# Performance work log

Hardware: AMD Instinct MI355X
Metric: run time of the kernel (lower is better)

## Reference

```python
import jax, jax.numpy as jnp
import numpy as np

B, C, H, W = 4, 16, 512, 512
OUT = 16
HID = 64
EPS = 1e-5


def _ln(x, g, b):
    mu = x.mean(-1, keepdims=True)
    v = x.var(-1, keepdims=True)
    return (x - mu) / jnp.sqrt(v + EPS) * g + b


def setup_inputs() -> dict:
    key = jax.random.key(0)
    ks = jax.random.split(key, 8)
    HW = H * W
    d = {}
    d['input'] = jax.random.normal(ks[0], (B, C, H, W), jnp.float32)
    d['W1'] = jax.random.normal(ks[1], (HID, HW), jnp.float32) * 0.01   # Linear1 weight [64, HW]
    d['b1'] = jnp.zeros((HID,), jnp.float32)
    d['ln1_g'] = jnp.ones((HID,), jnp.float32)
    d['ln1_b'] = jnp.zeros((HID,), jnp.float32)
    d['W2'] = jax.random.normal(ks[2], (HW, HID), jnp.float32) * 0.02   # Linear2 weight [HW, 64]
    d['b2'] = jnp.zeros((HW,), jnp.float32)
    d['ln2_g'] = jnp.ones((HW,), jnp.float32)
    d['ln2_b'] = jnp.zeros((HW,), jnp.float32)
    d['cw1'] = jax.random.normal(ks[3], (1, C, 1, 1), jnp.float32) * 0.1   # 1x1 conv C->1
    d['cb1'] = jnp.zeros((1,), jnp.float32)
    d['cw3'] = jax.random.normal(ks[4], (OUT, C, 3, 3), jnp.float32) * 0.05  # 3x3 conv C->OUT
    d['cb3'] = jnp.zeros((OUT,), jnp.float32)
    d['bn_g'] = jnp.ones((OUT,), jnp.float32)
    d['bn_b'] = jnp.zeros((OUT,), jnp.float32)
    return d


def reference(input, W1, b1, ln1_g, ln1_b, W2, b2, ln2_g, ln2_b, cw1, cb1, cw3, cb3, bn_g, bn_b):
    Bq, Cq, Hq, Wq = input.shape
    HW = Hq * Wq
    m = input.reshape(Bq, Cq, HW)
    # Linear1 -> LN -> ReLU  (per-channel over flattened spatial dim)
    h = jax.nn.relu(_ln(m @ W1.T + b1, ln1_g, ln1_b))            # [B, C, 64]
    # Linear2 -> LN -> ReLU
    m2 = jax.nn.relu(_ln(h @ W2.T + b2, ln2_g, ln2_b))           # [B, C, HW]
    m2 = m2.reshape(Bq, Cq, Hq, Wq)
    # 1x1 conv C -> 1
    score = jnp.einsum('bchw,oc->bohw', m2, cw1[:, :, 0, 0]) + cb1[:, None, None]  # [B,1,H,W]
    # keep_topk: ratio 0.25, no grad
    K = HW // 4
    flat = jax.lax.stop_gradient(score.reshape(Bq, HW))
    _, idx = jax.lax.top_k(flat, K)                               # [B, K]
    mask = jnp.zeros_like(flat).at[jnp.arange(Bq)[:, None], idx].set(1.0).reshape(Bq, 1, Hq, Wq)
    # boolean-mask gather: torch selects in ascending flat-index order
    idx_s = jnp.sort(idx, axis=1)                                 # [B, K]
    g = jnp.take_along_axis(m, idx_s[:, None, :], axis=2).reshape(Bq, Cq, Hq // 2, Wq // 2)
    # out_conv: 3x3 conv -> BatchNorm (batch stats, training mode) -> ReLU
    y = jax.lax.conv_general_dilated(g, cw3, (1, 1), [(1, 1), (1, 1)],
                                     dimension_numbers=('NCHW', 'OIHW', 'NCHW'))
    y = y + cb3[:, None, None]
    mu = y.mean((0, 2, 3), keepdims=True)
    v = y.var((0, 2, 3), keepdims=True)
    y = jax.nn.relu((y - mu) / jnp.sqrt(v + EPS) * bn_g[:, None, None] + bn_b[:, None, None])
    return (y, mask)
```

## Files before the change

kernel.cpp:

```cpp
#include <hip/hip_runtime.h>

#define HWN    262144
#define KSEL   65536
#define TIECAP 2048

#define OFF_H      0
#define OFF_DOT1   32768
#define OFF_G      65536
#define OFF_WBAR   98304
#define OFF_WB     98816
#define OFF_SB     99328
#define OFF_MU2    99360
#define OFF_ISIG2  99872
#define OFF_STATE  100384
#define OFF_HIST   100448
#define OFF_TIECNT 116832
#define OFF_CHCNT  116848
#define OFF_TIELST 116864
#define OFF_CHLST  149632
#define OFF_BCNT   182400
#define OFF_BOFF   186496
#define OFF_BNP    190592
#define OFF_BNC    452736
#define OFF_PART2  458752
#define OFF_HT     1015808
#define REGION2    1048576

#define PS_GRAM 4226
#define PS_DOT  4096

typedef double d4_t __attribute__((ext_vector_type(4)));
typedef float  f4v  __attribute__((ext_vector_type(4)));

__device__ __forceinline__ unsigned monokey(double s){
  unsigned long long b = (unsigned long long)__double_as_longlong(s);
  b = (b & 0x8000000000000000ULL) ? ~b : (b | 0x8000000000000000ULL);
  return (unsigned)(b >> 32);
}

__global__ void k_zero(unsigned* hist, unsigned* tiecnt, unsigned* chcnt, unsigned* state){
  int t = threadIdx.x;
  for (int i = t; i < 4096; i += 256) hist[i] = 0u;
  if (t < 4){
    tiecnt[t] = 0u; chcnt[t] = 0u;
    state[t*4+0] = 0u;
    state[t*4+1] = (unsigned)KSEL;
    state[t*4+2] = 0u;
    state[t*4+3] = 0u;
  }
}

__device__ __forceinline__ void st_tile(double* __restrict__ P, const d4_t& acc,
                                        const int* ri_, const int* ci_, int ai, int bi){
#pragma unroll
  for (int i = 0; i < 4; i++)
    P[(ai*16+ri_[i])*66 + bi*16 + ci_[i]] = acc[i];
}

#define GRAM_STEP(F0,F1,F2,F3,FB) { \
  double f0=(double)(F0), f1=(double)(F1), f2=(double)(F2), f3=(double)(F3); \
  if (w == 0){ \
    accA = __builtin_amdgcn_mfma_f64_16x16x4f64(f0, f0, accA, 0, 0, 0); \
    accB = __builtin_amdgcn_mfma_f64_16x16x4f64(f0, f1, accB, 0, 0, 0); \
    accC = __builtin_amdgcn_mfma_f64_16x16x4f64(f0, f2, accC, 0, 0, 0); \
  } else if (w == 1){ \
    accA = __builtin_amdgcn_mfma_f64_16x16x4f64(f0, f3, accA, 0, 0, 0); \
    accB = __builtin_amdgcn_mfma_f64_16x16x4f64(f1, f1, accB, 0, 0, 0); \
    accC = __builtin_amdgcn_mfma_f64_16x16x4f64(f1, f2, accC, 0, 0, 0); \
  } else if (w == 2){ \
    accA = __builtin_amdgcn_mfma_f64_16x16x4f64(f1, f3, accA, 0, 0, 0); \
    accB = __builtin_amdgcn_mfma_f64_16x16x4f64(f2, f2, accB, 0, 0, 0); \
    accC = __builtin_amdgcn_mfma_f64_16x16x4f64(f2, f3, accC, 0, 0, 0); \
  } else { \
    accA = __builtin_amdgcn_mfma_f64_16x16x4f64(f3, f3, accA, 0, 0, 0); \
    double bb = (double)(FB); \
    wbar0 += f0; wbar1 += f1; wbar2 += f2; wbar3 += f3; \
    wb0 += f0*bb; wb1 += f1*bb; wb2 += f2*bb; wb3 += f3*bb; \
    sb += bb; sb2 += bb*bb; \
  } }

#define G1_STEP(AV,B0,B1,B2,B3) { \
  _Pragma("unroll") \
  for (int t4 = 0; t4 < 4; t4++){ \
    double a = (double)(AV)[t4]; \
    acc0 = __builtin_amdgcn_mfma_f64_16x16x4f64(a, (double)(B0)[t4], acc0, 0, 0, 0); \
    acc1 = __builtin_amdgcn_mfma_f64_16x16x4f64(a, (double)(B1)[t4], acc1, 0, 0, 0); \
    acc2 = __builtin_amdgcn_mfma_f64_16x16x4f64(a, (double)(B2)[t4], acc2, 0, 0, 0); \
    acc3 = __builtin_amdgcn_mfma_f64_16x16x4f64(a, (double)(B3)[t4], acc3, 0, 0, 0); \
  } }

__global__ __launch_bounds__(256) void k_mm(const float* __restrict__ W2,
                                            const float* __restrict__ b2,
                                            const float* __restrict__ inp,
                                            const float* __restrict__ W1,
                                            double* __restrict__ partG,
                                            double* __restrict__ partD,
                                            int pPerBlk, int NBH){
  int t = threadIdx.x;
  int w = t >> 6, l = t & 63;
  int q = l >> 4, m = l & 15;
  if ((int)blockIdx.x < NBH){
    int p0 = blockIdx.x * pPerBlk;
    d4_t accA = {0.,0.,0.,0.}, accB = {0.,0.,0.,0.}, accC = {0.,0.,0.,0.};
    double wbar0=0., wbar1=0., wbar2=0., wbar3=0.;
    double wb0=0., wb1=0., wb2=0., wb3=0., sb=0., sb2=0.;
    const float* base = W2 + (size_t)(p0 + q)*64 + m;
    const float* b2p  = b2 + p0 + q;
    int nPair = pPerBlk >> 3;
    float gA0 = base[0], gA1 = base[16], gA2 = base[32], gA3 = base[48];
    float gAb = b2p[0];
    for (int i = 0; i < nPair; i++){
      float gB0 = base[256+0], gB1 = base[256+16], gB2 = base[256+32], gB3 = base[256+48];
      float gBb = b2p[4];
      GRAM_STEP(gA0, gA1, gA2, gA3, gAb)
      base += 512; b2p += 8;
      if (i + 1 < nPair){
        gA0 = base[0]; gA1 = base[16]; gA2 = base[32]; gA3 = base[48];
        gAb = b2p[0];
      }
      GRAM_STEP(gB0, gB1, gB2, gB3, gBb)
    }
    d4_t prD = {0.,0.,0.,0.}, pcD = {0.,0.,0.,0.};
    double rp = (double)(1 + m);
    prD = __builtin_amdgcn_mfma_f64_16x16x4f64(rp, 1.0, prD, 0, 0, 0);
    pcD = __builtin_amdgcn_mfma_f64_16x16x4f64(1.0, rp, pcD, 0, 0, 0);
    int ri_[4], ci_[4];
#pragma unroll
    for (int i = 0; i < 4; i++){
      ri_[i] = ((((int)prD[i]) >> 2) - 1) & 15;
      ci_[i] = ((((int)pcD[i]) >> 2) - 1) & 15;
    }
    double* P = partG + (size_t)blockIdx.x * PS_GRAM;
    if (w == 0){
      st_tile(P, accA, ri_, ci_, 0, 0); st_tile(P, accB, ri_, ci_, 0, 1);
      st_tile(P, accC, ri_, ci_, 0, 2);
    } else if (w == 1){
      st_tile(P, accA, ri_, ci_, 0, 3); st_tile(P, accB, ri_, ci_, 1, 1);
      st_tile(P, accC, ri_, ci_, 1, 2);
    } else if (w == 2){
      st_tile(P, accA, ri_, ci_, 1, 3); st_tile(P, accB, ri_, ci_, 2, 2);
      st_tile(P, accC, ri_, ci_, 2, 3);
    } else {
      st_tile(P, accA, ri_, ci_, 3, 3);
      wbar0 += __shfl_down(wbar0, 32); wbar1 += __shfl_down(wbar1, 32);
      wbar2 += __shfl_down(wbar2, 32); wbar3 += __shfl_down(wbar3, 32);
      wb0 += __shfl_down(wb0, 32); wb1 += __shfl_down(wb1, 32);
      wb2 += __shfl_down(wb2, 32); wb3 += __shfl_down(wb3, 32);
      sb += __shfl_down(sb, 32); sb2 += __shfl_down(sb2, 32);
      wbar0 += __shfl_down(wbar0, 16); wbar1 += __shfl_down(wbar1, 16);
      wbar2 += __shfl_down(wbar2, 16); wbar3 += __shfl_down(wbar3, 16);
      wb0 += __shfl_down(wb0, 16); wb1 += __shfl_down(wb1, 16);
      wb2 += __shfl_down(wb2, 16); wb3 += __shfl_down(wb3, 16);
      sb += __shfl_down(sb, 16); sb2 += __shfl_down(sb2, 16);
      if (l < 16){
        P[(m +  0)*66 + 64] = wb0;  P[(m +  0)*66 + 65] = wbar0;
        P[(m + 16)*66 + 64] = wb1;  P[(m + 16)*66 + 65] = wbar1;
        P[(m + 32)*66 + 64] = wb2;  P[(m + 32)*66 + 65] = wbar2;
        P[(m + 48)*66 + 64] = wb3;  P[(m + 48)*66 + 65] = wbar3;
      }
      if (l == 0){ P[4224] = sb2; P[4225] = sb; }
    }
  } else {
    int blk = (int)blockIdx.x - NBH;
    int p0 = blk * pPerBlk;
    d4_t acc0 = {0.,0.,0.,0.}, acc1 = {0.,0.,0.,0.};
    d4_t acc2 = {0.,0.,0.,0.}, acc3 = {0.,0.,0.,0.};
    const f4v* ap  = (const f4v*)(inp + (size_t)(w*16 + m)*HWN + p0 + q*4);
    const f4v* bp0 = (const f4v*)(W1  + (size_t)( 0 + m)*HWN + p0 + q*4);
    const f4v* bp1 = (const f4v*)(W1  + (size_t)(16 + m)*HWN + p0 + q*4);
    const f4v* bp2 = (const f4v*)(W1  + (size_t)(32 + m)*HWN + p0 + q*4);
    const f4v* bp3 = (const f4v*)(W1  + (size_t)(48 + m)*HWN + p0 + q*4);
    int nPair = pPerBlk >> 5;
    f4v avA = ap[0], b0A = bp0[0], b1A = bp1[0], b2A = bp2[0], b3A = bp3[0];
    for (int i = 0; i < nPair; i++){
      size_t x1 = (size_t)(2*i+1)*4;
      f4v avB = ap[x1], b0B = bp0[x1], b1B = bp1[x1], b2B = bp2[x1], b3B = bp3[x1];
      G1_STEP(avA, b0A, b1A, b2A, b3A)
      if (i + 1 < nPair){
        size_t x2 = (size_t)(2*i+2)*4;
        avA = ap[x2]; b0A = bp0[x2]; b1A = bp1[x2]; b2A = bp2[x2]; b3A = bp3[x2];
      }
      G1_STEP(avB, b0B, b1B, b2B, b3B)
    }
    d4_t prD = {0.,0.,0.,0.}, pcD = {0.,0.,0.,0.};
    double rp = (double)(1 + m);
    prD = __builtin_amdgcn_mfma_f64_16x16x4f64(rp, 1.0, prD, 0, 0, 0);
    pcD = __builtin_amdgcn_mfma_f64_16x16x4f64(1.0, rp, pcD, 0, 0, 0);
    double* P = partD + (size_t)blk * PS_DOT;
#pragma unroll
    for (int i = 0; i < 4; i++){
      int ri = ((((int)prD[i]) >> 2) - 1) & 15;
      int ci = ((((int)pcD[i]) >> 2) - 1) & 15;
      int r = w*16 + ri;
      P[r*64 +  0 + ci] = acc0[i];
      P[r*64 + 16 + ci] = acc1[i];
      P[r*64 + 32 + ci] = acc2[i];
      P[r*64 + 48 + ci] = acc3[i];
    }
  }
}

__global__ __launch_bounds__(256) void k_red1(const double* __restrict__ part,
                                              double* __restrict__ part2,
                                              int bPerGrp, int cnt){
  int nj = (cnt + 255) >> 8;
  int jc = blockIdx.x % nj;
  int grp = blockIdx.x / nj;
  int j = jc*256 + threadIdx.x;
  if (j >= cnt) return;
  const double* p = part + (size_t)grp * bPerGrp * cnt + j;
  double s0=0.0, s1=0.0, s2=0.0, s3=0.0;
  for (int b = 0; b < bPerGrp; b += 4){
    s0 += p[(size_t)(b+0)*cnt];
    s1 += p[(size_t)(b+1)*cnt];
    s2 += p[(size_t)(b+2)*cnt];
    s3 += p[(size_t)(b+3)*cnt];
  }
  part2[(size_t)grp*cnt + j] = (s0+s1) + (s2+s3);
}

__global__ void k_redgram2(const double* __restrict__ part2,
                           double* __restrict__ G, double* __restrict__ wb,
                           double* __restrict__ wbar, double* __restrict__ sbv){
  int j = blockIdx.x*256 + threadIdx.x;
  if (j >= PS_GRAM) return;
  int src = j;
  int r = 0, c = 0;
  if (j < 4224){
    r = j / 66; c = j % 66;
    if (c < 64){
      int rb = r >> 4, cb = c >> 4;
      if (cb < rb)
        src = ((cb*16 + (c & 15)) * 66) + rb*16 + (r & 15);
    }
  }
  double s = 0.0;
#pragma unroll
  for (int b = 0; b < 16; b++) s += part2[(size_t)b*PS_GRAM + src];
  if (j < 4224){
    if (c < 64) G[r*64 + c] = s;
    else if (c == 64) wb[r] = s;
    else wbar[r] = s;
  } else if (j == 4224) sbv[1] = s;
  else sbv[0] = s;
}

__global__ void k_reddot2(const double* __restrict__ part2, double* __restrict__ dot1){
  int j = blockIdx.x*256 + threadIdx.x;
  if (j >= PS_DOT) return;
  double s = 0.0;
#pragma unroll
  for (int b = 0; b < 16; b++) s += part2[(size_t)b*PS_DOT + j];
  dot1[j] = s;
}

__global__ void k_h(const double* __restrict__ dot1, const float* __restrict__ b1,
                    const float* __restrict__ g1, const float* __restrict__ b1l,
                    const double* __restrict__ wbar, const double* __restrict__ sbv,
                    double* __restrict__ h, double* __restrict__ hT,
                    double* __restrict__ mu2){
  int r = threadIdx.x;
  double m = 0.0;
  for (int k=0;k<64;k++) m += dot1[r*64+k] + (double)b1[k];
  m *= (1.0/64.0);
  double v = 0.0;
  for (int k=0;k<64;k++){ double d = dot1[r*64+k] + (double)b1[k] - m; v += d*d; }
  v *= (1.0/64.0);
  double inv = 1.0 / sqrt(v + 1e-5);
  double s2 = 0.0;
  for (int k=0;k<64;k++){
    double x = dot1[r*64+k] + (double)b1[k];
    double z = (x - m) * inv;
    double hv = z * (double)g1[k] + (double)b1l[k];
    hv = hv > 0.0 ? hv : 0.0;
    h[r*64+k] = hv;
    hT[k*64+r] = hv;
    s2 += hv * wbar[k];
  }
  mu2[r] = (s2 + sbv[0]) / (double)HWN;
}

__global__ void k_var2(const double* __restrict__ h, const double* __restrict__ G,
                       const double* __restrict__ wb, const double* __restrict__ sbv,
                       const double* __restrict__ mu2, double* __restrict__ isig2){
  int r = blockIdx.x, k = threadIdx.x;
  double hk = h[r*64+k];
  double v = 0.0;
  for (int l=0;l<64;l++) v += G[k*64+l] * h[r*64+l];
  double contrib = hk*v + 2.0*hk*wb[k];
  for (int o=32;o>0;o>>=1) contrib += __shfl_down(contrib, o);
  if (k == 0){
    double E2 = (contrib + sbv[1]) / (double)HWN;
    double mu = mu2[r];
    double var = E2 - mu*mu;
    isig2[r] = 1.0 / sqrt(var + 1e-5);
  }
}

#define SC_K(WF, KIDX) { \
  double w_ = (double)(WF); \
  const double* hp_ = hb + (KIDX)*64; \
  acc[0]+=hp_[0]*w_;  acc[1]+=hp_[1]*w_;  acc[2]+=hp_[2]*w_;  acc[3]+=hp_[3]*w_; \
  acc[4]+=hp_[4]*w_;  acc[5]+=hp_[5]*w_;  acc[6]+=hp_[6]*w_;  acc[7]+=hp_[7]*w_; \
  acc[8]+=hp_[8]*w_;  acc[9]+=hp_[9]*w_;  acc[10]+=hp_[10]*w_; acc[11]+=hp_[11]*w_; \
  acc[12]+=hp_[12]*w_; acc[13]+=hp_[13]*w_; acc[14]+=hp_[14]*w_; acc[15]+=hp_[15]*w_; }

__global__ __launch_bounds__(256) void k_score(const float* __restrict__ W2,
    const float* __restrict__ b2, const float* __restrict__ g2, const float* __restrict__ lb2,
    const float* __restrict__ cw1, const float* __restrict__ cb1,
    const double* __restrict__ hT, const double* __restrict__ mu2, const double* __restrict__ isg,
    double* __restrict__ score, unsigned* __restrict__ key, unsigned* __restrict__ hist){
  __shared__ unsigned lh[1024];
  int t = threadIdx.x;
  for (int i = t; i < 1024; i += 256) lh[i] = 0u;
  __syncthreads();
  int p = blockIdx.x*256 + t;
  float4 w4[16];
  const float4* wp = (const float4*)(W2 + (size_t)p*64);
#pragma unroll
  for (int i=0;i<16;i++) w4[i] = wp[i];
  double g2p = (double)g2[p], lb2p = (double)lb2[p], b2p = (double)b2[p];
  double cb = (double)cb1[0];
  for (int b = 0; b < 4; b++){
    double acc[16];
#pragma unroll
    for (int j=0;j<16;j++) acc[j]=0.0;
    const double* hb = hT + b*16;
#pragma unroll
    for (int k4=0;k4<16;k4++){
      float4 wv = w4[k4];
      SC_K(wv.x, (k4*4+0))
      SC_K(wv.y, (k4*4+1))
      SC_K(wv.z, (k4*4+2))
      SC_K(wv.w, (k4*4+3))
    }
    double sc = cb;
#pragma unroll
    for (int j=0;j<16;j++){
      int c = b*16 + j;
      double tv = acc[j] + b2p;
      double z = (tv - mu2[c]) * isg[c];
      double v = z * g2p + lb2p;
      v = v > 0.0 ? v : 0.0;
      sc += v * (double)cw1[j];
    }
    if (sc == 0.0) sc = 0.0;
    unsigned kk = monokey(sc);
    score[(size_t)b*HWN + p] = sc;
    key[(size_t)b*HWN + p] = kk;
    atomicAdd(&lh[b*256 + (kk >> 24)], 1u);
  }
  __syncthreads();
#pragma unroll
  for (int b = 0; b < 4; b++)
    atomicAdd(&hist[b*256 + t], lh[b*256 + t]);
}

__global__ void k_hist(const unsigned* __restrict__ key, const unsigned* __restrict__ state,
                       unsigned* __restrict__ hist, int pass){
  __shared__ unsigned lh[256];
  int t = threadIdx.x;
  int b = blockIdx.x >> 7, seg = blockIdx.x & 127;
  lh[t] = 0u;
  __syncthreads();
  unsigned pref = state[b*4+0];
  const unsigned* kb = key + (size_t)b*HWN + seg*2048;
  int shb = 24 - 8*pass;
#pragma unroll
  for (int i=0;i<8;i++){
    unsigned kk = kb[t + 256*i];
    bool ok = (pass == 0) || ((kk >> (32 - 8*pass)) == pref);
    if (ok) atomicAdd(&lh[(kk >> shb) & 255u], 1u);
  }
  __syncthreads();
  atomicAdd(&hist[(pass*4 + b)*256 + t], lh[t]);
}

__global__ void k_scan(unsigned* __restrict__ state, const unsigned* __restrict__ hist, int pass){
  __shared__ unsigned ls[4*256];
  int t = threadIdx.x;
  int b = t >> 8, j = t & 255;
  unsigned cnt = hist[(pass*4 + b)*256 + j];
  int q = 255 - j;
  ls[b*256 + q] = cnt;
  __syncthreads();
  for (int o=1;o<256;o<<=1){
    unsigned v = (q >= o) ? ls[b*256 + q - o] : 0u;
    __syncthreads();
    ls[b*256 + q] += v;
    __syncthreads();
  }
  unsigned need = state[b*4+1];
  unsigned pref = state[b*4+0];
  unsigned GT = (j == 255) ? 0u : ls[b*256 + (254 - j)];
  unsigned GE = ls[b*256 + (255 - j)];
  if (GT < need && need <= GE){
    unsigned npref = (pref << 8) | (unsigned)j;
    state[b*4+0] = npref;
    state[b*4+1] = need - GT;
    if (pass == 3){ state[b*4+2] = npref; state[b*4+3] = need - GT; }
  }
}

__global__ __launch_bounds__(256) void k_mask(const unsigned* __restrict__ key,
    const unsigned* __restrict__ state, float* __restrict__ outM,
    unsigned* __restrict__ bcnt, unsigned* __restrict__ tiecnt, unsigned* __restrict__ tielist){
  __shared__ int red[256];
  int t = threadIdx.x;
  int b = blockIdx.x >> 8, seg = blockIdx.x & 255;
  unsigned T = state[b*4+2];
  int p0 = seg*1024 + t*4;
  size_t base = (size_t)b*HWN + p0;
  uint4 kk = *((const uint4*)(key + base));
  float4 mv; int cnt = 0;
  { int s = kk.x > T; mv.x = s ? 1.f : 0.f; cnt += s;
    if (kk.x == T){ unsigned ti = atomicAdd(&tiecnt[b],1u); if (ti < TIECAP) tielist[b*TIECAP+ti] = (unsigned)(p0+0); } }
  { int s = kk.y > T; mv.y = s ? 1.f : 0.f; cnt += s;
    if (kk.y == T){ unsigned ti = atomicAdd(&tiecnt[b],1u); if (ti < TIECAP) tielist[b*TIECAP+ti] = (unsigned)(p0+1); } }
  { int s = kk.z > T; mv.z = s ? 1.f : 0.f; cnt += s;
    if (kk.z == T){ unsigned ti = atomicAdd(&tiecnt[b],1u); if (ti < TIECAP) tielist[b*TIECAP+ti] = (unsigned)(p0+2); } }
  { int s = kk.w > T; mv.w = s ? 1.f : 0.f; cnt += s;
    if (kk.w == T){ unsigned ti = atomicAdd(&tiecnt[b],1u); if (ti < TIECAP) tielist[b*TIECAP+ti] = (unsigned)(p0+3); } }
  *((float4*)(outM + base)) = mv;
  red[t] = cnt;
  __syncthreads();
  for (int o=128;o>0;o>>=1){ if (t < o) red[t] += red[t+o]; __syncthreads(); }
  if (t == 0) bcnt[b*256 + seg] = (unsigned)red[0];
}

__global__ __launch_bounds__(256) void k_ties(const unsigned* __restrict__ state,
    const unsigned* __restrict__ tiecnt, const unsigned* __restrict__ tielist,
    const double* __restrict__ score, float* __restrict__ outM,
    unsigned* __restrict__ chcnt, unsigned* __restrict__ chlist){
  __shared__ double ssc[TIECAP];
  __shared__ unsigned spp[TIECAP];
  __shared__ unsigned skeep[TIECAP];
  int b = blockIdx.x, t = threadIdx.x;
  unsigned tc = tiecnt[b];
  int n = (int)(tc < (unsigned)TIECAP ? tc : (unsigned)TIECAP);
  unsigned nt = state[b*4+3];
  for (int i=t;i<n;i+=256){
    unsigned p = tielist[b*TIECAP+i];
    spp[i] = p; ssc[i] = score[(size_t)b*HWN + p];
  }
  __syncthreads();
  for (int i=t;i<n;i+=256){
    double si = ssc[i]; unsigned pi = spp[i]; int r = 0;
    for (int j=0;j<n;j++){
      double sj = ssc[j]; unsigned pj = spp[j];
      if (sj > si || (sj == si && pj < pi)) r++;
    }
    skeep[i] = (r < (int)nt) ? 1u : 0u;
  }
  __syncthreads();
  for (int i=t;i<n;i+=256){
    if (skeep[i]){
      unsigned pi = spp[i]; int r2 = 0;
      for (int j=0;j<n;j++) if (skeep[j] && spp[j] < pi) r2++;
      chlist[b*TIECAP + r2] = pi;
      outM[(size_t)b*HWN + pi] = 1.0f;
    }
  }
  if (t == 0){
    unsigned c = ((unsigned)n < nt) ? (unsigned)n : nt;
    chcnt[b] = c;
  }
}

__global__ void k_scanblk(const unsigned* __restrict__ bcnt, unsigned* __restrict__ boff){
  __shared__ unsigned ls[1024];
  int t = threadIdx.x; int b = t >> 8, j = t & 255;
  unsigned own = bcnt[b*256 + j];
  ls[t] = own;
  __syncthreads();
  for (int o=1;o<256;o<<=1){
    unsigned v = (j >= o) ? ls[b*256 + j - o] : 0u;
    __syncthreads();
    ls[t] += v;
    __syncthreads();
  }
  boff[b*256 + j] = ls[t] - own;
}

__device__ __forceinline__ void gath_one(unsigned kv, int p, unsigned T,
    const unsigned* __restrict__ cl, unsigned nch, unsigned base, int& run,
    const float* __restrict__ inp, float* __restrict__ g, int b){
  int isGT = kv > T;
  int isCh = 0;
  if (kv == T && nch > 0u){
    for (unsigned j=0;j<nch;j++) if (cl[j] == (unsigned)p){ isCh = 1; break; }
  }
  if (isGT | isCh){
    unsigned adj = 0;
    for (unsigned j=0;j<nch;j++) adj += (cl[j] < (unsigned)p) ? 1u : 0u;
    unsigned rank = base + (unsigned)run + adj;
#pragma unroll
    for (int c=0;c<16;c++)
      g[(size_t)(b*16+c)*KSEL + rank] = inp[(size_t)(b*16+c)*HWN + p];
  }
  run += isGT;
}

__global__ __launch_bounds__(256) void k_gather(const unsigned* __restrict__ key,
    const unsigned* __restrict__ state, const unsigned* __restrict__ boff,
    const unsigned* __restrict__ chcnt, const unsigned* __restrict__ chlist,
    const float* __restrict__ inp, float* __restrict__ g){
  __shared__ int wt[4];
  int t = threadIdx.x;
  int b = blockIdx.x >> 8, seg = blockIdx.x & 255;
  unsigned T = state[b*4+2];
  int p0 = seg*1024 + t*4;
  uint4 kk = *((const uint4*)(key + (size_t)b*HWN + p0));
  int s0 = kk.x > T, s1 = kk.y > T, s2 = kk.z > T, s3 = kk.w > T;
  int cnt = s0 + s1 + s2 + s3;
  int l = t & 63;
  int incl = cnt;
#pragma unroll
  for (int o=1;o<64;o<<=1){ int v = __shfl_up(incl, o); if (l >= o) incl += v; }
  int w = t >> 6;
  if (l == 63) wt[w] = incl;
  __syncthreads();
  int wex = 0;
#pragma unroll
  for (int i=0;i<4;i++) if (i < w) wex += wt[i];
  int exth = incl - cnt;
  unsigned base = boff[b*256 + seg] + (unsigned)wex + (unsigned)exth;
  unsigned nch = chcnt[b];
  const unsigned* cl = chlist + b*TIECAP;
  int run = 0;
  gath_one(kk.x, p0+0, T, cl, nch, base, run, inp, g, b);
  gath_one(kk.y, p0+1, T, cl, nch, base, run, inp, g, b);
  gath_one(kk.z, p0+2, T, cl, nch, base, run, inp, g, b);
  gath_one(kk.w, p0+3, T, cl, nch, base, run, inp, g, b);
}

__global__ __launch_bounds__(256) void k_conv(const float* __restrict__ g,
    const float* __restrict__ cw3, const float* __restrict__ cb3,
    float* __restrict__ outY, double* __restrict__ bnp){
  __shared__ float wsm[2304];
  __shared__ float it[18*18];
  __shared__ double red[16][4][2];
  int t = threadIdx.x;
  int b = blockIdx.x >> 8, tile = blockIdx.x & 255;
  int ty0 = (tile >> 4) * 16, tx0 = (tile & 15) * 16;
  int tx = t & 15, ty = t >> 4;
#pragma unroll
  for (int i=0;i<9;i++){ int j = t + 256*i; if (j < 2304) wsm[j] = cw3[j]; }
  float acc[16];
#pragma unroll
  for (int i=0;i<16;i++) acc[i] = 0.f;
  for (int ic=0; ic<16; ic++){
    __syncthreads();
    for (int j=t;j<324;j+=256){
      int gy = ty0 - 1 + j/18, gx = tx0 - 1 + (j%18);
      float v = 0.f;
      if (gy >= 0 && gy < 256 && gx >= 0 && gx < 256)
        v = g[(size_t)(b*16+ic)*KSEL + gy*256 + gx];
      it[j] = v;
    }
    __syncthreads();
#pragma unroll
    for (int ky=0;ky<3;ky++)
#pragma unroll
      for (int kx=0;kx<3;kx++){
        float v = it[(ty+ky)*18 + tx+kx];
#pragma unroll
        for (int oc=0;oc<16;oc++) acc[oc] += v * wsm[oc*144 + ic*9 + ky*3 + kx];
      }
  }
  int w = t >> 6, l = t & 63;
  for (int oc=0;oc<16;oc++){
    float yv = acc[oc] + cb3[oc];
    outY[(size_t)(b*16+oc)*KSEL + (ty0+ty)*256 + tx0+tx] = yv;
    double s = (double)yv, q = (double)yv*(double)yv;
    for (int o=32;o>0;o>>=1){ s += __shfl_down(s, o); q += __shfl_down(q, o); }
    if (l == 0){ red[oc][w][0] = s; red[oc][w][1] = q; }
  }
  __syncthreads();
  if (t < 16){
    double s=0.0, q=0.0;
    for (int w2=0;w2<4;w2++){ s += red[t][w2][0]; q += red[t][w2][1]; }
    bnp[(size_t)blockIdx.x*32 + t*2]   = s;
    bnp[(size_t)blockIdx.x*32 + t*2+1] = q;
  }
}

__global__ void k_bnred(const double* __restrict__ bnp, const float* __restrict__ bng,
                        const float* __restrict__ bnb, float* __restrict__ bnc){
  __shared__ double red[16][16][2];
  int t = threadIdx.x; int oc = t >> 4, sl = t & 15;
  double s = 0.0, q = 0.0;
  for (int i=0;i<64;i++){
    int blk = sl*64 + i;
    s += bnp[(size_t)blk*32 + oc*2];
    q += bnp[(size_t)blk*32 + oc*2+1];
  }
  red[oc][sl][0] = s; red[oc][sl][1] = q;
  __syncthreads();
  if (t < 16){
    double S=0.0, Q=0.0;
    for (int i=0;i<16;i++){ S += red[t][i][0]; Q += red[t][i][1]; }
    double N = 262144.0;
    double mu = S/N, var = Q/N - mu*mu;
    double inv = 1.0 / sqrt(var + 1e-5);
    double a = (double)bng[t] * inv;
    double bsh = (double)bnb[t] - mu*a;
    bnc[t*2] = (float)a; bnc[t*2+1] = (float)bsh;
  }
}

__global__ void k_bnapply(float* __restrict__ outY, const float* __restrict__ bnc){
  int i = blockIdx.x*256 + threadIdx.x;
  float4 v = ((float4*)outY)[i];
  int oc = (i >> 14) & 15;
  float a = bnc[oc*2], bsh = bnc[oc*2+1];
  v.x = fmaxf(v.x*a + bsh, 0.f);
  v.y = fmaxf(v.y*a + bsh, 0.f);
  v.z = fmaxf(v.z*a + bsh, 0.f);
  v.w = fmaxf(v.w*a + bsh, 0.f);
  ((float4*)outY)[i] = v;
}

extern "C" void kernel_launch(void* const* d_in, const int* in_sizes, int n_in,
                              void* d_out, int out_size, void* d_ws, size_t ws_size,
                              hipStream_t stream){
  const float* inp  = (const float*)d_in[0];
  const float* W1   = (const float*)d_in[1];
  const float* b1   = (const float*)d_in[2];
  const float* g1   = (const float*)d_in[3];
  const float* b1l  = (const float*)d_in[4];
  const float* W2   = (const float*)d_in[5];
  const float* b2   = (const float*)d_in[6];
  const float* g2   = (const float*)d_in[7];
  const float* lb2  = (const float*)d_in[8];
  const float* cw1  = (const float*)d_in[9];
  const float* cb1  = (const float*)d_in[10];
  const float* cw3  = (const float*)d_in[11];
  const float* cb3  = (const float*)d_in[12];
  const float* bng  = (const float*)d_in[13];
  const float* bnb  = (const float*)d_in[14];
  (void)in_sizes; (void)n_in; (void)out_size;

  char* ws = (char*)d_ws;
  float* outY = (float*)d_out;
  float* outM = outY + 4194304;

  size_t need512  = (size_t)REGION2 + 512ull*4352*8 + 16777216ull;
  int NBH = (ws_size >= need512) ? 512 : 128;
  int pPerBlk = HWN / NBH;
  int bPerGrp = NBH / 16;

  double*  partG  = (double*)(ws + REGION2);
  double*  partD  = (double*)(ws + REGION2 + (size_t)NBH*PS_GRAM*8);
  double*  score  = (double*)(ws + REGION2);
  unsigned* key   = (unsigned*)(ws + REGION2 + 8388608ull);
  float*   gbuf   = (float*)(ws + REGION2 + 12582912ull);
  double*  hbuf   = (double*)(ws + OFF_H);
  double*  hTbuf  = (double*)(ws + OFF_HT);
  double*  dot1   = (double*)(ws + OFF_DOT1);
  double*  G      = (double*)(ws + OFF_G);
  double*  wbar   = (double*)(ws + OFF_WBAR);
  double*  wb     = (double*)(ws + OFF_WB);
  double*  sbv    = (double*)(ws + OFF_SB);
  double*  mu2    = (double*)(ws + OFF_MU2);
  double*  isg    = (double*)(ws + OFF_ISIG2);
  unsigned* state = (unsigned*)(ws + OFF_STATE);
  unsigned* hist  = (unsigned*)(ws + OFF_HIST);
  unsigned* tiecnt= (unsigned*)(ws + OFF_TIECNT);
  unsigned* chcnt = (unsigned*)(ws + OFF_CHCNT);
  unsigned* tielist=(unsigned*)(ws + OFF_TIELST);
  unsigned* chlist= (unsigned*)(ws + OFF_CHLST);
  unsigned* bcnt  = (unsigned*)(ws + OFF_BCNT);
  unsigned* boff  = (unsigned*)(ws + OFF_BOFF);
  double*  bnp    = (double*)(ws + OFF_BNP);
  float*   bnc    = (float*)(ws + OFF_BNC);
  double*  part2  = (double*)(ws + OFF_PART2);

  k_zero<<<1, 256, 0, stream>>>(hist, tiecnt, chcnt, state);
  k_mm<<<2*NBH, 256, 0, stream>>>(W2, b2, inp, W1, partG, partD, pPerBlk, NBH);
  k_red1<<<17*16, 256, 0, stream>>>(partG, part2, bPerGrp, PS_GRAM);
  k_redgram2<<<17, 256, 0, stream>>>(part2, G, wb, wbar, sbv);
  k_red1<<<16*16, 256, 0, stream>>>(partD, part2, bPerGrp, PS_DOT);
  k_reddot2<<<16, 256, 0, stream>>>(part2, dot1);
  k_h<<<1, 64, 0, stream>>>(dot1, b1, g1, b1l, wbar, sbv, hbuf, hTbuf, mu2);
  k_var2<<<64, 64, 0, stream>>>(hbuf, G, wb, sbv, mu2, isg);
  k_score<<<1024, 256, 0, stream>>>(W2, b2, g2, lb2, cw1, cb1, hTbuf, mu2, isg, score, key, hist);
  k_scan<<<1, 1024, 0, stream>>>(state, hist, 0);
  for (int pass = 1; pass < 4; pass++){
    k_hist<<<512, 256, 0, stream>>>(key, state, hist, pass);
    k_scan<<<1, 1024, 0, stream>>>(state, hist, pass);
  }
  k_mask<<<1024, 256, 0, stream>>>(key, state, outM, bcnt, tiecnt, tielist);
  k_ties<<<4, 256, 0, stream>>>(state, tiecnt, tielist, score, outM, chcnt, chlist);
  k_scanblk<<<1, 1024, 0, stream>>>(bcnt, boff);
  k_gather<<<1024, 256, 0, stream>>>(key, state, boff, chcnt, chlist, inp, gbuf);
  k_conv<<<1024, 256, 0, stream>>>(gbuf, cw3, cb3, outY, bnp);
  k_bnred<<<1, 256, 0, stream>>>(bnp, bng, bnb, bnc);
  k_bnapply<<<4096, 256, 0, stream>>>(outY, bnc);
}
```

Before: 387.3 us.

## Fold scan kernels into last-block epilogues and merge small reduction kernels

Removes the separate single-block scan kernels (radix scans, block-offset scan) by having the last finishing block of k_score, k_hist and k_mask, detected with an atomic done counter, perform the prefix scan and state update. The two-level partial reductions are replaced by single kernels that each reduce all partials. The h/LN and variance kernels are merged into one 256-thread kernel that reads the raw Gram buffer directly. This cuts the launch count and the serialized tiny kernels, at the cost of atomic counters, threadfences and a serialized tail in the last block.

```diff
diff --git a/kernel.cpp b/kernel.cpp
--- a/kernel.cpp
+++ b/kernel.cpp
@@ -4,12 +4,8 @@
 #define KSEL   65536
 #define TIECAP 2048
 
-#define OFF_H      0
 #define OFF_DOT1   32768
 #define OFF_G      65536
-#define OFF_WBAR   98304
-#define OFF_WB     98816
-#define OFF_SB     99328
 #define OFF_MU2    99360
 #define OFF_ISIG2  99872
 #define OFF_STATE  100384
@@ -22,7 +18,7 @@
 #define OFF_BOFF   186496
 #define OFF_BNP    190592
 #define OFF_BNC    452736
-#define OFF_PART2  458752
+#define OFF_DONE   452864
 #define OFF_HT     1015808
 #define REGION2    1048576
 
@@ -38,9 +34,11 @@
   return (unsigned)(b >> 32);
 }
 
-__global__ void k_zero(unsigned* hist, unsigned* tiecnt, unsigned* chcnt, unsigned* state){
+__global__ void k_zero(unsigned* hist, unsigned* tiecnt, unsigned* chcnt,
+                       unsigned* state, unsigned* done){
   int t = threadIdx.x;
   for (int i = t; i < 4096; i += 256) hist[i] = 0u;
+  if (t < 8) done[t] = 0u;
   if (t < 4){
     tiecnt[t] = 0u; chcnt[t] = 0u;
     state[t*4+0] = 0u;
@@ -200,100 +198,91 @@
   }
 }
 
-__global__ __launch_bounds__(256) void k_red1(const double* __restrict__ part,
-                                              double* __restrict__ part2,
-                                              int bPerGrp, int cnt){
-  int nj = (cnt + 255) >> 8;
-  int jc = blockIdx.x % nj;
-  int grp = blockIdx.x / nj;
-  int j = jc*256 + threadIdx.x;
-  if (j >= cnt) return;
-  const double* p = part + (size_t)grp * bPerGrp * cnt + j;
-  double s0=0.0, s1=0.0, s2=0.0, s3=0.0;
-  for (int b = 0; b < bPerGrp; b += 4){
-    s0 += p[(size_t)(b+0)*cnt];
-    s1 += p[(size_t)(b+1)*cnt];
-    s2 += p[(size_t)(b+2)*cnt];
-    s3 += p[(size_t)(b+3)*cnt];
-  }
-  part2[(size_t)grp*cnt + j] = (s0+s1) + (s2+s3);
-}
-
-__global__ void k_redgram2(const double* __restrict__ part2,
-                           double* __restrict__ G, double* __restrict__ wb,
-                           double* __restrict__ wbar, double* __restrict__ sbv){
-  int j = blockIdx.x*256 + threadIdx.x;
-  if (j >= PS_GRAM) return;
-  int src = j;
-  int r = 0, c = 0;
-  if (j < 4224){
-    r = j / 66; c = j % 66;
-    if (c < 64){
-      int rb = r >> 4, cb = c >> 4;
-      if (cb < rb)
-        src = ((cb*16 + (c & 15)) * 66) + rb*16 + (r & 15);
-    }
-  }
-  double s = 0.0;
-#pragma unroll
-  for (int b = 0; b < 16; b++) s += part2[(size_t)b*PS_GRAM + src];
-  if (j < 4224){
-    if (c < 64) G[r*64 + c] = s;
-    else if (c == 64) wb[r] = s;
-    else wbar[r] = s;
-  } else if (j == 4224) sbv[1] = s;
-  else sbv[0] = s;
-}
-
-__global__ void k_reddot2(const double* __restrict__ part2, double* __restrict__ dot1){
-  int j = blockIdx.x*256 + threadIdx.x;
-  if (j >= PS_DOT) return;
-  double s = 0.0;
-#pragma unroll
-  for (int b = 0; b < 16; b++) s += part2[(size_t)b*PS_DOT + j];
-  dot1[j] = s;
-}
-
-__global__ void k_h(const double* __restrict__ dot1, const float* __restrict__ b1,
-                    const float* __restrict__ g1, const float* __restrict__ b1l,
-                    const double* __restrict__ wbar, const double* __restrict__ sbv,
-                    double* __restrict__ h, double* __restrict__ hT,
-                    double* __restrict__ mu2){
-  int r = threadIdx.x;
+__global__ __launch_bounds__(256) void k_redG(const double* __restrict__ part,
+                                              double* __restrict__ Gl, int NBH){
+  __shared__ double red[4][64];
+  int t = threadIdx.x;
+  int s = t >> 6, jl = t & 63;
+  int j = blockIdx.x*64 + jl;
+  double sum = 0.0;
+  if (j < PS_GRAM)
+    for (int i = s; i < NBH; i += 4) sum += part[(size_t)i*PS_GRAM + j];
+  red[s][jl] = sum;
+  __syncthreads();
+  if (s == 0 && j < PS_GRAM)
+    Gl[j] = (red[0][jl]+red[1][jl]) + (red[2][jl]+red[3][jl]);
+}
+
+__global__ __launch_bounds__(256) void k_redD(const double* __restrict__ part,
+                                              double* __restrict__ dot1, int NBH){
+  __shared__ double red[4][64];
+  int t = threadIdx.x;
+  int s = t >> 6, jl = t & 63;
+  int j = blockIdx.x*64 + jl;
+  double sum = 0.0;
+  for (int i = s; i < NBH; i += 4) sum += part[(size_t)i*PS_DOT + j];
+  red[s][jl] = sum;
+  __syncthreads();
+  if (s == 0)
+    dot1[j] = (red[0][jl]+red[1][jl]) + (red[2][jl]+red[3][jl]);
+}
+
+__global__ __launch_bounds__(256) void k_hv(const double* __restrict__ dot1,
+    const float* __restrict__ b1, const float* __restrict__ g1,
+    const float* __restrict__ b1l, const double* __restrict__ Gl,
+    double* __restrict__ hT, double* __restrict__ mu2, double* __restrict__ isg){
+  __shared__ double hsh[64*64];
+  __shared__ double mu2s[64];
+  int t = threadIdx.x;
+  int r = t >> 2, kt = t & 3;
+  int lane = t & 63;
+  int gbase = lane & ~3;
   double m = 0.0;
-  for (int k=0;k<64;k++) m += dot1[r*64+k] + (double)b1[k];
+  for (int k = kt*16; k < kt*16+16; k++) m += dot1[r*64+k] + (double)b1[k];
+  m += __shfl_down(m, 1); m += __shfl_down(m, 2);
+  m = __shfl(m, gbase);
   m *= (1.0/64.0);
-  double v = 0.0;
-  for (int k=0;k<64;k++){ double d = dot1[r*64+k] + (double)b1[k] - m; v += d*d; }
-  v *= (1.0/64.0);
-  double inv = 1.0 / sqrt(v + 1e-5);
+  double vv = 0.0;
+  for (int k = kt*16; k < kt*16+16; k++){
+    double d = dot1[r*64+k] + (double)b1[k] - m; vv += d*d;
+  }
+  vv += __shfl_down(vv, 1); vv += __shfl_down(vv, 2);
+  vv = __shfl(vv, gbase);
+  double inv = 1.0 / sqrt(vv*(1.0/64.0) + 1e-5);
   double s2 = 0.0;
-  for (int k=0;k<64;k++){
+  for (int k = kt*16; k < kt*16+16; k++){
     double x = dot1[r*64+k] + (double)b1[k];
     double z = (x - m) * inv;
-    double hv = z * (double)g1[k] + (double)b1l[k];
+    double hv = z*(double)g1[k] + (double)b1l[k];
     hv = hv > 0.0 ? hv : 0.0;
-    h[r*64+k] = hv;
+    hsh[r*64+k] = hv;
     hT[k*64+r] = hv;
-    s2 += hv * wbar[k];
-  }
-  mu2[r] = (s2 + sbv[0]) / (double)HWN;
-}
-
-__global__ void k_var2(const double* __restrict__ h, const double* __restrict__ G,
-                       const double* __restrict__ wb, const double* __restrict__ sbv,
-                       const double* __restrict__ mu2, double* __restrict__ isig2){
-  int r = blockIdx.x, k = threadIdx.x;
-  double hk = h[r*64+k];
-  double v = 0.0;
-  for (int l=0;l<64;l++) v += G[k*64+l] * h[r*64+l];
-  double contrib = hk*v + 2.0*hk*wb[k];
-  for (int o=32;o>0;o>>=1) contrib += __shfl_down(contrib, o);
-  if (k == 0){
-    double E2 = (contrib + sbv[1]) / (double)HWN;
-    double mu = mu2[r];
+    s2 += hv * Gl[k*66+65];
+  }
+  s2 += __shfl_down(s2, 1); s2 += __shfl_down(s2, 2);
+  if (kt == 0){
+    double mu = (s2 + Gl[4225]) / (double)HWN;
+    mu2s[r] = mu; mu2[r] = mu;
+  }
+  __syncthreads();
+  double contrib = 0.0;
+  for (int k = kt; k < 64; k += 4){
+    double hk = hsh[r*64+k];
+    double v = 0.0;
+    int kb = k >> 4;
+    for (int l2 = 0; l2 < 64; l2++){
+      int lb = l2 >> 4;
+      double gv = (kb <= lb) ? Gl[k*66 + l2] : Gl[l2*66 + k];
+      v += gv * hsh[r*64+l2];
+    }
+    contrib += hk*v + 2.0*hk*Gl[k*66+64];
+  }
+  contrib += __shfl_down(contrib, 1); contrib += __shfl_down(contrib, 2);
+  if (kt == 0){
+    double E2 = (contrib + Gl[4224]) / (double)HWN;
+    double mu = mu2s[r];
     double var = E2 - mu*mu;
-    isig2[r] = 1.0 / sqrt(var + 1e-5);
+    isg[r] = 1.0 / sqrt(var + 1e-5);
   }
 }
 
@@ -309,8 +298,10 @@
     const float* __restrict__ b2, const float* __restrict__ g2, const float* __restrict__ lb2,
     const float* __restrict__ cw1, const float* __restrict__ cb1,
     const double* __restrict__ hT, const double* __restrict__ mu2, const double* __restrict__ isg,
-    double* __restrict__ score, unsigned* __restrict__ key, unsigned* __restrict__ hist){
+    double* __restrict__ score, unsigned* __restrict__ key,
+    unsigned* __restrict__ hist, unsigned* __restrict__ state, unsigned* __restrict__ done){
   __shared__ unsigned lh[1024];
+  __shared__ unsigned lastf;
   int t = threadIdx.x;
   for (int i = t; i < 1024; i += 256) lh[i] = 0u;
   __syncthreads();
@@ -354,11 +345,38 @@
 #pragma unroll
   for (int b = 0; b < 4; b++)
     atomicAdd(&hist[b*256 + t], lh[b*256 + t]);
-}
-
-__global__ void k_hist(const unsigned* __restrict__ key, const unsigned* __restrict__ state,
-                       unsigned* __restrict__ hist, int pass){
+  __threadfence();
+  __syncthreads();
+  if (t == 0) lastf = (atomicAdd(&done[0], 1u) == (unsigned)(gridDim.x - 1)) ? 1u : 0u;
+  __syncthreads();
+  if (lastf){
+    for (int bb = 0; bb < 4; bb++){
+      unsigned cnt = atomicAdd(&hist[bb*256 + t], 0u);
+      int q = 255 - t;
+      lh[q] = cnt;
+      __syncthreads();
+      for (int o = 1; o < 256; o <<= 1){
+        unsigned v = (q >= o) ? lh[q - o] : 0u;
+        __syncthreads();
+        lh[q] += v;
+        __syncthreads();
+      }
+      unsigned GT = (t == 255) ? 0u : lh[254 - t];
+      unsigned GE = lh[255 - t];
+      if (GT < (unsigned)KSEL && (unsigned)KSEL <= GE){
+        state[bb*4+0] = (unsigned)t;
+        state[bb*4+1] = (unsigned)KSEL - GT;
+      }
+      __syncthreads();
+    }
+  }
+}
+
+__global__ void k_hist(const unsigned* __restrict__ key, unsigned* __restrict__ state,
+                       unsigned* __restrict__ hist, int pass, unsigned* __restrict__ done){
   __shared__ unsigned lh[256];
+  __shared__ unsigned ls2[256];
+  __shared__ unsigned lastf;
   int t = threadIdx.x;
   int b = blockIdx.x >> 7, seg = blockIdx.x & 127;
   lh[t] = 0u;
@@ -369,43 +387,49 @@
 #pragma unroll
   for (int i=0;i<8;i++){
     unsigned kk = kb[t + 256*i];
-    bool ok = (pass == 0) || ((kk >> (32 - 8*pass)) == pref);
+    bool ok = ((kk >> (32 - 8*pass)) == pref);
     if (ok) atomicAdd(&lh[(kk >> shb) & 255u], 1u);
   }
   __syncthreads();
   atomicAdd(&hist[(pass*4 + b)*256 + t], lh[t]);
-}
-
-__global__ void k_scan(unsigned* __restrict__ state, const unsigned* __restrict__ hist, int pass){
-  __shared__ unsigned ls[4*256];
-  int t = threadIdx.x;
-  int b = t >> 8, j = t & 255;
-  unsigned cnt = hist[(pass*4 + b)*256 + j];
-  int q = 255 - j;
-  ls[b*256 + q] = cnt;
-  __syncthreads();
-  for (int o=1;o<256;o<<=1){
-    unsigned v = (q >= o) ? ls[b*256 + q - o] : 0u;
-    __syncthreads();
-    ls[b*256 + q] += v;
-    __syncthreads();
-  }
-  unsigned need = state[b*4+1];
-  unsigned pref = state[b*4+0];
-  unsigned GT = (j == 255) ? 0u : ls[b*256 + (254 - j)];
-  unsigned GE = ls[b*256 + (255 - j)];
-  if (GT < need && need <= GE){
-    unsigned npref = (pref << 8) | (unsigned)j;
-    state[b*4+0] = npref;
-    state[b*4+1] = need - GT;
-    if (pass == 3){ state[b*4+2] = npref; state[b*4+3] = need - GT; }
+  __threadfence();
+  __syncthreads();
+  if (t == 0) lastf = (atomicAdd(&done[pass], 1u) == (unsigned)(gridDim.x - 1)) ? 1u : 0u;
+  __syncthreads();
+  if (lastf){
+    for (int bb = 0; bb < 4; bb++){
+      unsigned cnt = atomicAdd(&hist[(pass*4 + bb)*256 + t], 0u);
+      int q = 255 - t;
+      ls2[q] = cnt;
+      __syncthreads();
+      for (int o = 1; o < 256; o <<= 1){
+        unsigned v = (q >= o) ? ls2[q - o] : 0u;
+        __syncthreads();
+        ls2[q] += v;
+        __syncthreads();
+      }
+      unsigned need = state[bb*4+1];
+      unsigned pr   = state[bb*4+0];
+      unsigned GT = (t == 255) ? 0u : ls2[254 - t];
+      unsigned GE = ls2[255 - t];
+      if (GT < need && need <= GE){
+        unsigned np = (pr << 8) | (unsigned)t;
+        state[bb*4+0] = np;
+        state[bb*4+1] = need - GT;
+        if (pass == 3){ state[bb*4+2] = np; state[bb*4+3] = need - GT; }
+      }
+      __syncthreads();
+    }
   }
 }
 
 __global__ __launch_bounds__(256) void k_mask(const unsigned* __restrict__ key,
     const unsigned* __restrict__ state, float* __restrict__ outM,
-    unsigned* __restrict__ bcnt, unsigned* __restrict__ tiecnt, unsigned* __restrict__ tielist){
+    unsigned* __restrict__ bcnt, unsigned* __restrict__ tiecnt, unsigned* __restrict__ tielist,
+    unsigned* __restrict__ boff, unsigned* __restrict__ done){
   __shared__ int red[256];
+  __shared__ unsigned lsb[256];
+  __shared__ unsigned lastf;
   int t = threadIdx.x;
   int b = blockIdx.x >> 8, seg = blockIdx.x & 255;
   unsigned T = state[b*4+2];
@@ -426,6 +450,25 @@
   __syncthreads();
   for (int o=128;o>0;o>>=1){ if (t < o) red[t] += red[t+o]; __syncthreads(); }
   if (t == 0) bcnt[b*256 + seg] = (unsigned)red[0];
+  __threadfence();
+  __syncthreads();
+  if (t == 0) lastf = (atomicAdd(&done[4], 1u) == (unsigned)(gridDim.x - 1)) ? 1u : 0u;
+  __syncthreads();
+  if (lastf){
+    for (int bb = 0; bb < 4; bb++){
+      unsigned own = atomicAdd(&bcnt[bb*256 + t], 0u);
+      lsb[t] = own;
+      __syncthreads();
+      for (int o = 1; o < 256; o <<= 1){
+        unsigned v = (t >= o) ? lsb[t - o] : 0u;
+        __syncthreads();
+        lsb[t] += v;
+        __syncthreads();
+      }
+      boff[bb*256 + t] = lsb[t] - own;
+      __syncthreads();
+    }
+  }
 }
 
 __global__ __launch_bounds__(256) void k_ties(const unsigned* __restrict__ state,
@@ -465,21 +508,6 @@
     unsigned c = ((unsigned)n < nt) ? (unsigned)n : nt;
     chcnt[b] = c;
   }
-}
-
-__global__ void k_scanblk(const unsigned* __restrict__ bcnt, unsigned* __restrict__ boff){
-  __shared__ unsigned ls[1024];
-  int t = threadIdx.x; int b = t >> 8, j = t & 255;
-  unsigned own = bcnt[b*256 + j];
-  ls[t] = own;
-  __syncthreads();
-  for (int o=1;o<256;o<<=1){
-    unsigned v = (j >= o) ? ls[b*256 + j - o] : 0u;
-    __syncthreads();
-    ls[t] += v;
-    __syncthreads();
-  }
-  boff[b*256 + j] = ls[t] - own;
 }
 
 __device__ __forceinline__ void gath_one(unsigned kv, int p, unsigned T,
@@ -648,20 +676,15 @@
   size_t need512  = (size_t)REGION2 + 512ull*4352*8 + 16777216ull;
   int NBH = (ws_size >= need512) ? 512 : 128;
   int pPerBlk = HWN / NBH;
-  int bPerGrp = NBH / 16;
 
   double*  partG  = (double*)(ws + REGION2);
   double*  partD  = (double*)(ws + REGION2 + (size_t)NBH*PS_GRAM*8);
   double*  score  = (double*)(ws + REGION2);
   unsigned* key   = (unsigned*)(ws + REGION2 + 8388608ull);
   float*   gbuf   = (float*)(ws + REGION2 + 12582912ull);
-  double*  hbuf   = (double*)(ws + OFF_H);
+  double*  Gl     = (double*)(ws + OFF_G);
   double*  hTbuf  = (double*)(ws + OFF_HT);
   double*  dot1   = (double*)(ws + OFF_DOT1);
-  double*  G      = (double*)(ws + OFF_G);
-  double*  wbar   = (double*)(ws + OFF_WBAR);
-  double*  wb     = (double*)(ws + OFF_WB);
-  double*  sbv    = (double*)(ws + OFF_SB);
   double*  mu2    = (double*)(ws + OFF_MU2);
   double*  isg    = (double*)(ws + OFF_ISIG2);
   unsigned* state = (unsigned*)(ws + OFF_STATE);
@@ -674,25 +697,19 @@
   unsigned* boff  = (unsigned*)(ws + OFF_BOFF);
   double*  bnp    = (double*)(ws + OFF_BNP);
   float*   bnc    = (float*)(ws + OFF_BNC);
-  double*  part2  = (double*)(ws + OFF_PART2);
-
-  k_zero<<<1, 256, 0, stream>>>(hist, tiecnt, chcnt, state);
+  unsigned* done  = (unsigned*)(ws + OFF_DONE);
+
+  k_zero<<<1, 256, 0, stream>>>(hist, tiecnt, chcnt, state, done);
   k_mm<<<2*NBH, 256, 0, stream>>>(W2, b2, inp, W1, partG, partD, pPerBlk, NBH);
-  k_red1<<<17*16, 256, 0, stream>>>(partG, part2, bPerGrp, PS_GRAM);
-  k_redgram2<<<17, 256, 0, stream>>>(part2, G, wb, wbar, sbv);
-  k_red1<<<16*16, 256, 0, stream>>>(partD, part2, bPerGrp, PS_DOT);
-  k_reddot2<<<16, 256, 0, stream>>>(part2, dot1);
-  k_h<<<1, 64, 0, stream>>>(dot1, b1, g1, b1l, wbar, sbv, hbuf, hTbuf, mu2);
-  k_var2<<<64, 64, 0, stream>>>(hbuf, G, wb, sbv, mu2, isg);
-  k_score<<<1024, 256, 0, stream>>>(W2, b2, g2, lb2, cw1, cb1, hTbuf, mu2, isg, score, key, hist);
-  k_scan<<<1, 1024, 0, stream>>>(state, hist, 0);
-  for (int pass = 1; pass < 4; pass++){
-    k_hist<<<512, 256, 0, stream>>>(key, state, hist, pass);
-    k_scan<<<1, 1024, 0, stream>>>(state, hist, pass);
-  }
-  k_mask<<<1024, 256, 0, stream>>>(key, state, outM, bcnt, tiecnt, tielist);
+  k_redG<<<(PS_GRAM + 63)/64, 256, 0, stream>>>(partG, Gl, NBH);
+  k_redD<<<PS_DOT/64, 256, 0, stream>>>(partD, dot1, NBH);
+  k_hv<<<1, 256, 0, stream>>>(dot1, b1, g1, b1l, Gl, hTbuf, mu2, isg);
+  k_score<<<1024, 256, 0, stream>>>(W2, b2, g2, lb2, cw1, cb1, hTbuf, mu2, isg,
+                                    score, key, hist, state, done);
+  for (int pass = 1; pass < 4; pass++)
+    k_hist<<<512, 256, 0, stream>>>(key, state, hist, pass, done);
+  k_mask<<<1024, 256, 0, stream>>>(key, state, outM, bcnt, tiecnt, tielist, boff, done);
   k_ties<<<4, 256, 0, stream>>>(state, tiecnt, tielist, score, outM, chcnt, chlist);
-  k_scanblk<<<1, 1024, 0, stream>>>(bcnt, boff);
   k_gather<<<1024, 256, 0, stream>>>(key, state, boff, chcnt, chlist, inp, gbuf);
   k_conv<<<1024, 256, 0, stream>>>(gbuf, cw3, cb3, outY, bnp);
   k_bnred<<<1, 256, 0, stream>>>(bnp, bng, bnb, bnc);
```

New measurement: 692.3 us. 78.8% more time.

## Fuse hidden LN and variance kernels; move first radix histogram out of score kernel

Applied to the files above, without the earlier changes.

Merges the single-block k_h and the 64-block k_var2 into one 256-thread kernel that keeps h in shared memory and splits each row's work across four lanes with shuffle reductions. This removes one launch and the global round trip for h. It also drops the shared-memory histogram and atomics from k_score and computes the pass-0 histogram with an extra k_hist launch instead. The trade is a lighter score kernel against one more full read of the key array. The fused kernel runs on a single block, so the Gram-based variance step now uses only one CU.

```diff
diff --git a/kernel.cpp b/kernel.cpp
--- a/kernel.cpp
+++ b/kernel.cpp
@@ -254,46 +254,60 @@
   dot1[j] = s;
 }
 
-__global__ void k_h(const double* __restrict__ dot1, const float* __restrict__ b1,
-                    const float* __restrict__ g1, const float* __restrict__ b1l,
-                    const double* __restrict__ wbar, const double* __restrict__ sbv,
-                    double* __restrict__ h, double* __restrict__ hT,
-                    double* __restrict__ mu2){
-  int r = threadIdx.x;
+__global__ __launch_bounds__(256) void k_hv(const double* __restrict__ dot1,
+    const float* __restrict__ b1, const float* __restrict__ g1,
+    const float* __restrict__ b1l, const double* __restrict__ G,
+    const double* __restrict__ wbar, const double* __restrict__ wb,
+    const double* __restrict__ sbv, double* __restrict__ hT,
+    double* __restrict__ mu2, double* __restrict__ isg){
+  __shared__ double hsh[64*64];
+  __shared__ double mu2s[64];
+  int t = threadIdx.x;
+  int r = t >> 2, kt = t & 3;
+  int lane = t & 63;
+  int gbase = lane & ~3;
   double m = 0.0;
-  for (int k=0;k<64;k++) m += dot1[r*64+k] + (double)b1[k];
+  for (int k = kt*16; k < kt*16+16; k++) m += dot1[r*64+k] + (double)b1[k];
+  m += __shfl_down(m, 1); m += __shfl_down(m, 2);
+  m = __shfl(m, gbase);
   m *= (1.0/64.0);
-  double v = 0.0;
-  for (int k=0;k<64;k++){ double d = dot1[r*64+k] + (double)b1[k] - m; v += d*d; }
-  v *= (1.0/64.0);
-  double inv = 1.0 / sqrt(v + 1e-5);
+  double vv = 0.0;
+  for (int k = kt*16; k < kt*16+16; k++){
+    double d = dot1[r*64+k] + (double)b1[k] - m; vv += d*d;
+  }
+  vv += __shfl_down(vv, 1); vv += __shfl_down(vv, 2);
+  vv = __shfl(vv, gbase);
+  double inv = 1.0 / sqrt(vv*(1.0/64.0) + 1e-5);
   double s2 = 0.0;
-  for (int k=0;k<64;k++){
+  for (int k = kt*16; k < kt*16+16; k++){
     double x = dot1[r*64+k] + (double)b1[k];
     double z = (x - m) * inv;
-    double hv = z * (double)g1[k] + (double)b1l[k];
+    double hv = z*(double)g1[k] + (double)b1l[k];
     hv = hv > 0.0 ? hv : 0.0;
-    h[r*64+k] = hv;
+    hsh[r*64+k] = hv;
     hT[k*64+r] = hv;
     s2 += hv * wbar[k];
   }
-  mu2[r] = (s2 + sbv[0]) / (double)HWN;
-}
-
-__global__ void k_var2(const double* __restrict__ h, const double* __restrict__ G,
-                       const double* __restrict__ wb, const double* __restrict__ sbv,
-                       const double* __restrict__ mu2, double* __restrict__ isig2){
-  int r = blockIdx.x, k = threadIdx.x;
-  double hk = h[r*64+k];
-  double v = 0.0;
-  for (int l=0;l<64;l++) v += G[k*64+l] * h[r*64+l];
-  double contrib = hk*v + 2.0*hk*wb[k];
-  for (int o=32;o>0;o>>=1) contrib += __shfl_down(contrib, o);
-  if (k == 0){
+  s2 += __shfl_down(s2, 1); s2 += __shfl_down(s2, 2);
+  if (kt == 0){
+    double mu = (s2 + sbv[0]) / (double)HWN;
+    mu2s[r] = mu; mu2[r] = mu;
+  }
+  __syncthreads();
+  double contrib = 0.0;
+  for (int k = kt; k < 64; k += 4){
+    double hk = hsh[r*64+k];
+    double v = 0.0;
+    for (int l2 = 0; l2 < 64; l2++)
+      v += G[k*64 + l2] * hsh[r*64+l2];
+    contrib += hk*v + 2.0*hk*wb[k];
+  }
+  contrib += __shfl_down(contrib, 1); contrib += __shfl_down(contrib, 2);
+  if (kt == 0){
     double E2 = (contrib + sbv[1]) / (double)HWN;
-    double mu = mu2[r];
+    double mu = mu2s[r];
     double var = E2 - mu*mu;
-    isig2[r] = 1.0 / sqrt(var + 1e-5);
+    isg[r] = 1.0 / sqrt(var + 1e-5);
   }
 }
 
@@ -309,11 +323,8 @@
     const float* __restrict__ b2, const float* __restrict__ g2, const float* __restrict__ lb2,
     const float* __restrict__ cw1, const float* __restrict__ cb1,
     const double* __restrict__ hT, const double* __restrict__ mu2, const double* __restrict__ isg,
-    double* __restrict__ score, unsigned* __restrict__ key, unsigned* __restrict__ hist){
-  __shared__ unsigned lh[1024];
-  int t = threadIdx.x;
-  for (int i = t; i < 1024; i += 256) lh[i] = 0u;
-  __syncthreads();
+    double* __restrict__ score, unsigned* __restrict__ key){
+  int t = threadIdx.x;
   int p = blockIdx.x*256 + t;
   float4 w4[16];
   const float4* wp = (const float4*)(W2 + (size_t)p*64);
@@ -345,15 +356,9 @@
       sc += v * (double)cw1[j];
     }
     if (sc == 0.0) sc = 0.0;
-    unsigned kk = monokey(sc);
     score[(size_t)b*HWN + p] = sc;
-    key[(size_t)b*HWN + p] = kk;
-    atomicAdd(&lh[b*256 + (kk >> 24)], 1u);
-  }
-  __syncthreads();
-#pragma unroll
-  for (int b = 0; b < 4; b++)
-    atomicAdd(&hist[b*256 + t], lh[b*256 + t]);
+    key[(size_t)b*HWN + p] = monokey(sc);
+  }
 }
 
 __global__ void k_hist(const unsigned* __restrict__ key, const unsigned* __restrict__ state,
@@ -655,7 +660,6 @@
   double*  score  = (double*)(ws + REGION2);
   unsigned* key   = (unsigned*)(ws + REGION2 + 8388608ull);
   float*   gbuf   = (float*)(ws + REGION2 + 12582912ull);
-  double*  hbuf   = (double*)(ws + OFF_H);
   double*  hTbuf  = (double*)(ws + OFF_HT);
   double*  dot1   = (double*)(ws + OFF_DOT1);
   double*  G      = (double*)(ws + OFF_G);
@@ -682,11 +686,9 @@
   k_redgram2<<<17, 256, 0, stream>>>(part2, G, wb, wbar, sbv);
   k_red1<<<16*16, 256, 0, stream>>>(partD, part2, bPerGrp, PS_DOT);
   k_reddot2<<<16, 256, 0, stream>>>(part2, dot1);
-  k_h<<<1, 64, 0, stream>>>(dot1, b1, g1, b1l, wbar, sbv, hbuf, hTbuf, mu2);
-  k_var2<<<64, 64, 0, stream>>>(hbuf, G, wb, sbv, mu2, isg);
-  k_score<<<1024, 256, 0, stream>>>(W2, b2, g2, lb2, cw1, cb1, hTbuf, mu2, isg, score, key, hist);
-  k_scan<<<1, 1024, 0, stream>>>(state, hist, 0);
-  for (int pass = 1; pass < 4; pass++){
+  k_hv<<<1, 256, 0, stream>>>(dot1, b1, g1, b1l, G, wbar, wb, sbv, hTbuf, mu2, isg);
+  k_score<<<1024, 256, 0, stream>>>(W2, b2, g2, lb2, cw1, cb1, hTbuf, mu2, isg, score, key);
+  for (int pass = 0; pass < 4; pass++){
     k_hist<<<512, 256, 0, stream>>>(key, state, hist, pass);
     k_scan<<<1, 1024, 0, stream>>>(state, hist, pass);
   }
```

Result: slower. 420.4 us (+8.6%).
